# Performance work log

Hardware: AMD Instinct MI355X
Metric: run time of the kernel (lower is better)

Reference implementation:

```python
import jax, jax.numpy as jnp
import numpy as np

NUM_GROUPS = 5
EPS = 1e-5
QB = 128.0  # 2**(8-1) for b=8 activation quantization


def _binarize_weights_groupwise(W):
    """Sign-binarize W group-wise along out-feature dim, STE on backward.
    Faithful to torch: rows beyond num_groups*group_size remain zero."""
    n_out = W.shape[0]
    gs = n_out // NUM_GROUPS
    Wb = jnp.zeros_like(W)
    for g in range(NUM_GROUPS):  # small fixed loop (5 groups)
        wg = W[g * gs:(g + 1) * gs]
        z = wg - wg.mean()
        # STE: forward = sign(z), backward = identity w.r.t. z
        ste = z + jax.lax.stop_gradient(jnp.sign(z) - z)
        Wb = Wb.at[g * gs:(g + 1) * gs].set(ste)
    return Wb


def _quantize_activations_groupwise(x):
    """8-bit absmax quantization group-wise along dim 0 (batch), per torch code."""
    n = x.shape[0]
    gs = n // NUM_GROUPS
    xq = jnp.zeros_like(x)
    for g in range(NUM_GROUPS):
        ag = x[g * gs:(g + 1) * gs]
        gamma = jnp.max(jnp.abs(ag))
        xq = xq.at[g * gs:(g + 1) * gs].set(
            jnp.clip(ag * QB / (gamma + EPS), -QB + EPS, QB - EPS))
    return xq


def _bitlinear(x, W, b):
    Wb = _binarize_weights_groupwise(W)
    y = jnp.einsum('btc,oc->bto', x, Wb) + b
    return _quantize_activations_groupwise(y)


def setup_inputs() -> dict:
    key = jax.random.key(0)
    k1, k2, k3, k4, k5 = jax.random.split(key, 5)
    B, T, C = 10, 2048, 384
    H = 4 * C
    lim1 = 1.0 / np.sqrt(C)
    lim2 = 1.0 / np.sqrt(H)
    x = jax.random.normal(k1, (B, T, C), dtype=jnp.float32)
    W1 = jax.random.uniform(k2, (H, C), minval=-lim1, maxval=lim1, dtype=jnp.float32)
    b1 = jax.random.uniform(k3, (H,), minval=-lim1, maxval=lim1, dtype=jnp.float32)
    W2 = jax.random.uniform(k4, (C, H), minval=-lim2, maxval=lim2, dtype=jnp.float32)
    b2 = jax.random.uniform(k5, (C,), minval=-lim2, maxval=lim2, dtype=jnp.float32)
    return {"x": x, "W1": W1, "b1": b1, "W2": W2, "b2": b2}


def reference(x, W1, b1, W2, b2):
    h = _bitlinear(x, W1, b1)           # [B,T,4C], quantized to [-128,128]
    h = jax.nn.gelu(h, approximate=False)  # torch nn.GELU default is exact
    out = _bitlinear(h, W2, b2)         # [B,T,C]
    return out  # nn.Dropout is identity in eval/reference mode
```

## Files before the change

kernel.cpp:

```cpp
#include <hip/hip_runtime.h>
#include <cstdint>
#include <cstddef>

#define THREADS 256
#define NB 8

typedef float f32x4 __attribute__((ext_vector_type(4)));
typedef __bf16 bf16x8 __attribute__((ext_vector_type(8)));
typedef __bf16 bf16x4 __attribute__((ext_vector_type(4)));

__device__ __forceinline__ void gload_lds16(const void* g, void* l) {
    auto gp = (const __attribute__((address_space(1))) unsigned int*)(unsigned long long)(uintptr_t)g;
    auto lp = (__attribute__((address_space(3))) unsigned int*)(unsigned int)(uintptr_t)l;
    __builtin_amdgcn_global_load_lds(gp, lp, 16, 0, 0);
}

__device__ __forceinline__ float gelu_fast(float f) {
    const float z = f * 0.70710678118654752f;
    const float az = fabsf(z);
    const float t = __builtin_amdgcn_rcpf(fmaf(0.3275911f, az, 1.0f));
    float poly = fmaf(1.061405429f, t, -1.453152027f);
    poly = fmaf(poly, t, 1.421413741f);
    poly = fmaf(poly, t, -0.284496736f);
    poly = fmaf(poly, t, 0.254829592f);
    poly *= t;
    const float e = __builtin_amdgcn_exp2f(-az * az * 1.44269504088896f);
    float erfv = fmaf(-poly, e, 1.0f);
    erfv = copysignf(erfv, z);
    return 0.5f * f * (1.0f + erfv);
}

__global__ void prep_a(const float* __restrict__ x, __bf16* __restrict__ xb,
                       const float* __restrict__ W1, const float* __restrict__ W2,
                       float* __restrict__ partials, int epg1, int epg2,
                       unsigned int* __restrict__ gzero) {
    const int blk = blockIdx.x, tid = threadIdx.x;
    if (blk < 80) {
        const int y = blk >> 3, b = blk & 7;
        if (blk == 0 && tid < 16) gzero[tid] = 0u;
        const int epg = (y < 5) ? epg1 : epg2;
        const float* Wg = (y < 5) ? (W1 + (size_t)y * epg1)
                                  : (W2 + (size_t)(y - 5) * epg2);
        const int chunk4 = epg / (4 * NB);
        const float* base = Wg + (size_t)b * chunk4 * 4;
        float s = 0.f;
        for (int i = tid; i < chunk4; i += THREADS) {
            f32x4 v = *reinterpret_cast<const f32x4*>(base + 4 * (size_t)i);
            s += (v[0] + v[1]) + (v[2] + v[3]);
        }
        __shared__ float red[THREADS];
        red[tid] = s;
        __syncthreads();
        for (int off = THREADS / 2; off > 0; off >>= 1) {
            if (tid < off) red[tid] += red[tid + off];
            __syncthreads();
        }
        if (tid == 0) partials[y * NB + b] = red[0];
        return;
    }
    const int i = (blk - 80) * THREADS + tid;
    f32x4 v = *reinterpret_cast<const f32x4*>(x + 4 * (size_t)i);
    bf16x4 o;
    o[0] = (__bf16)v[0]; o[1] = (__bf16)v[1];
    o[2] = (__bf16)v[2]; o[3] = (__bf16)v[3];
    *reinterpret_cast<bf16x4*>(xb + 4 * (size_t)i) = o;
}

__global__ void prep_b(const float* __restrict__ W1, __bf16* __restrict__ W1b,
                       const float* __restrict__ W2, __bf16* __restrict__ W2b,
                       const float* __restrict__ psums,
                       int epg1, int tail1, int epg2, int tail2) {
    int r = blockIdx.x;
    const int tid = threadIdx.x;
    const float* W; __bf16* Wb; const float* ps; int epg, tail;
    if (r <= 40) { W = W1; Wb = W1b; ps = psums;      epg = epg1; tail = tail1; }
    else { r -= 41; W = W2; Wb = W2b; ps = psums + 40; epg = epg2; tail = tail2; }
    if (r == 40) {
        __bf16* og = Wb + (size_t)5 * epg;
        for (int i = tid; i < tail; i += THREADS) og[i] = (__bf16)0.f;
        return;
    }
    const int g = r >> 3, b = r & 7;
    float total = 0.f;
#pragma unroll
    for (int j = 0; j < NB; ++j) total += ps[g * NB + j];
    const float mean = total / (float)epg;
    const int chunk4 = epg / (4 * NB);
    const size_t off0 = (size_t)g * epg + (size_t)b * chunk4 * 4;
    const float* base = W + off0;
    __bf16* ob = Wb + off0;
    for (int i = tid; i < chunk4; i += THREADS) {
        f32x4 v = *reinterpret_cast<const f32x4*>(base + 4 * (size_t)i);
        bf16x4 o;
#pragma unroll
        for (int j = 0; j < 4; ++j) {
            const float z = v[j] - mean;
            o[j] = (__bf16)((z > 0.f) ? 1.f : ((z < 0.f) ? -1.f : 0.f));
        }
        *reinterpret_cast<bf16x4*>(ob + 4 * (size_t)i) = o;
    }
}

__global__ __launch_bounds__(512, 2)
void gemm1_bt(const __bf16* __restrict__ A, const __bf16* __restrict__ Bw,
              const float* __restrict__ bias, __bf16* __restrict__ outp,
              unsigned int* __restrict__ gmax, int M, int N, int K,
              int GN, int nwg) {
    constexpr int BM = 256, BN_ = 256, BK = 64, NF = 4;
    constexpr int ABYTES = BM * BK * 2;
    constexpr int BBYTES = BN_ * BK * 2;
    __shared__ __attribute__((aligned(16))) char lds[2 * (ABYTES + BBYTES)];

    const int tid = threadIdx.x;
    const int wave = tid >> 6, lane = tid & 63;
    const int l15 = lane & 15, l4 = lane >> 4;
    const int wr = wave >> 2, wc = wave & 3;

    const int cpx = nwg >> 3;
    const int orig = (blockIdx.x & 7) * cpx + (blockIdx.x >> 3);
    const int bm = orig / GN, bn = orig % GN;

    const __bf16* Ab = A + (size_t)bm * BM * K;
    const __bf16* Bb = Bw + (size_t)bn * BN_ * K;
    const int NT = K / BK;

    f32x4 acc[8][NF];
#pragma unroll
    for (int m = 0; m < 8; ++m)
#pragma unroll
        for (int n = 0; n < NF; ++n)
            acc[m][n] = f32x4{0.f, 0.f, 0.f, 0.f};

    auto STAGE = [&](int t) {
        const int k0 = t * BK;
        char* ab = lds + (t & 1) * (ABYTES + BBYTES);
        char* bb = ab + ABYTES;
#pragma unroll
        for (int j = 0; j < 4; ++j) {
            const int q = j * 8192 + tid * 16;
            const int lr = q >> 7;
            const int s = ((q >> 4) & 7) ^ (lr & 7);
            gload_lds16(Ab + (size_t)lr * K + k0 + s * 8, ab + q);
        }
#pragma unroll
        for (int j = 0; j < 4; ++j) {
            const int q = j * 8192 + tid * 16;
            const int lr = q >> 7;
            const int s = ((q >> 4) & 7) ^ (lr & 7);
            gload_lds16(Bb + (size_t)lr * K + k0 + s * 8, bb + q);
        }
    };

    STAGE(0);
    asm volatile("s_waitcnt vmcnt(0)" ::: "memory");
    __syncthreads();

    for (int t = 0; t < NT; ++t) {
        if (t + 1 < NT) STAGE(t + 1);
        const char* ab = lds + (t & 1) * (ABYTES + BBYTES);
        const char* bb = ab + ABYTES;
#pragma unroll
        for (int kk = 0; kk < 2; ++kk) {
            bf16x8 af[8], bfv[NF];
#pragma unroll
            for (int m = 0; m < 8; ++m) {
                const int r = wr * 128 + m * 16 + l15;
                const int sp = (kk * 4 + l4) ^ (r & 7);
                af[m] = *reinterpret_cast<const bf16x8*>(ab + r * 128 + sp * 16);
            }
#pragma unroll
            for (int n = 0; n < NF; ++n) {
                const int r = wc * 64 + n * 16 + l15;
                const int sp = (kk * 4 + l4) ^ (r & 7);
                bfv[n] = *reinterpret_cast<const bf16x8*>(bb + r * 128 + sp * 16);
            }
#pragma unroll
            for (int m = 0; m < 8; ++m)
#pragma unroll
                for (int n = 0; n < NF; ++n)
                    acc[m][n] = __builtin_amdgcn_mfma_f32_16x16x32_bf16(
                        bfv[n], af[m], acc[m][n], 0, 0, 0);
        }
        asm volatile("s_waitcnt vmcnt(0)" ::: "memory");
        __syncthreads();
    }

    const int rowb = bm * BM + wr * 128;
    const int colb = bn * BN_ + wc * 64;
    float lmax = 0.f;
#pragma unroll
    for (int n = 0; n < NF; ++n) {
        const f32x4 bv = *reinterpret_cast<const f32x4*>(bias + colb + n * 16 + l4 * 4);
#pragma unroll
        for (int m = 0; m < 8; ++m) {
            const int row = rowb + m * 16 + l15;
            bf16x4 o;
#pragma unroll
            for (int r = 0; r < 4; ++r) {
                const float v = acc[m][n][r] + bv[r];
                lmax = fmaxf(lmax, fabsf(v));
                o[r] = (__bf16)v;
            }
            *reinterpret_cast<bf16x4*>(
                &outp[(size_t)row * N + colb + n * 16 + l4 * 4]) = o;
        }
    }
#pragma unroll
    for (int off = 32; off > 0; off >>= 1)
        lmax = fmaxf(lmax, __shfl_down(lmax, off, 64));
    float* wredmax = (float*)lds;
    if (lane == 0) wredmax[wave] = lmax;
    __syncthreads();
    if (tid == 0) {
        float bmax = wredmax[0];
#pragma unroll
        for (int w = 1; w < 8; ++w) bmax = fmaxf(bmax, wredmax[w]);
        atomicMax(gmax + (bm * BM) / 4096, __float_as_uint(bmax));
    }
}

__global__ __launch_bounds__(512, 2)
void gemm2_bt(const __bf16* __restrict__ A, const __bf16* __restrict__ Bw,
              const float* __restrict__ bias, float* __restrict__ outp,
              unsigned int* __restrict__ gmax, int M, int N, int K,
              int GN, int nwg) {
    constexpr int BM = 256, BN_ = 128, BK = 64, NF = 2;
    constexpr int ABYTES = BM * BK * 2;
    constexpr int BBYTES = BN_ * BK * 2;
    __shared__ __attribute__((aligned(16))) char lds[2 * (ABYTES + BBYTES)];

    const int tid = threadIdx.x;
    const int wave = tid >> 6, lane = tid & 63;
    const int l15 = lane & 15, l4 = lane >> 4;
    const int wr = wave >> 2, wc = wave & 3;

    const int cpx = nwg >> 3;
    const int orig = (blockIdx.x & 7) * cpx + (blockIdx.x >> 3);
    const int bm = orig / GN, bn = orig % GN;

    const __bf16* Ab = A + (size_t)bm * BM * K;
    const __bf16* Bb = Bw + (size_t)bn * BN_ * K;
    const int NT = K / BK;

    f32x4 acc[8][NF];
#pragma unroll
    for (int m = 0; m < 8; ++m)
#pragma unroll
        for (int n = 0; n < NF; ++n)
            acc[m][n] = f32x4{0.f, 0.f, 0.f, 0.f};

    auto STAGE = [&](int t) {
        const int k0 = t * BK;
        char* ab = lds + (t & 1) * (ABYTES + BBYTES);
        char* bb = ab + ABYTES;
#pragma unroll
        for (int j = 0; j < 4; ++j) {
            const int q = j * 8192 + tid * 16;
            const int lr = q >> 7;
            const int s = ((q >> 4) & 7) ^ (lr & 7);
            gload_lds16(Ab + (size_t)lr * K + k0 + s * 8, ab + q);
        }
#pragma unroll
        for (int j = 0; j < 2; ++j) {
            const int q = j * 8192 + tid * 16;
            const int lr = q >> 7;
            const int s = ((q >> 4) & 7) ^ (lr & 7);
            gload_lds16(Bb + (size_t)lr * K + k0 + s * 8, bb + q);
        }
    };

    STAGE(0);
    asm volatile("s_waitcnt vmcnt(0)" ::: "memory");
    __syncthreads();

    for (int t = 0; t < NT; ++t) {
        if (t + 1 < NT) STAGE(t + 1);
        const char* ab = lds + (t & 1) * (ABYTES + BBYTES);
        const char* bb = ab + ABYTES;
#pragma unroll
        for (int kk = 0; kk < 2; ++kk) {
            bf16x8 af[8], bfv[NF];
#pragma unroll
            for (int m = 0; m < 8; ++m) {
                const int r = wr * 128 + m * 16 + l15;
                const int sp = (kk * 4 + l4) ^ (r & 7);
                af[m] = *reinterpret_cast<const bf16x8*>(ab + r * 128 + sp * 16);
            }
#pragma unroll
            for (int n = 0; n < NF; ++n) {
                const int r = wc * 32 + n * 16 + l15;
                const int sp = (kk * 4 + l4) ^ (r & 7);
                bfv[n] = *reinterpret_cast<const bf16x8*>(bb + r * 128 + sp * 16);
            }
#pragma unroll
            for (int m = 0; m < 8; ++m)
#pragma unroll
                for (int n = 0; n < NF; ++n)
                    acc[m][n] = __builtin_amdgcn_mfma_f32_16x16x32_bf16(
                        bfv[n], af[m], acc[m][n], 0, 0, 0);
        }
        asm volatile("s_waitcnt vmcnt(0)" ::: "memory");
        __syncthreads();
    }

    const int rowb = bm * BM + wr * 128;
    const int colb = bn * BN_ + wc * 32;
    float lmax = 0.f;
#pragma unroll
    for (int n = 0; n < NF; ++n) {
        const f32x4 bv = *reinterpret_cast<const f32x4*>(bias + colb + n * 16 + l4 * 4);
#pragma unroll
        for (int m = 0; m < 8; ++m) {
            const int row = rowb + m * 16 + l15;
            f32x4 o;
#pragma unroll
            for (int r = 0; r < 4; ++r) {
                o[r] = acc[m][n][r] + bv[r];
                lmax = fmaxf(lmax, fabsf(o[r]));
            }
            *reinterpret_cast<f32x4*>(
                &outp[(size_t)row * N + colb + n * 16 + l4 * 4]) = o;
        }
    }
#pragma unroll
    for (int off = 32; off > 0; off >>= 1)
        lmax = fmaxf(lmax, __shfl_down(lmax, off, 64));
    float* wredmax = (float*)lds;
    if (lane == 0) wredmax[wave] = lmax;
    __syncthreads();
    if (tid == 0) {
        float bmax = wredmax[0];
#pragma unroll
        for (int w = 1; w < 8; ++w) bmax = fmaxf(bmax, wredmax[w]);
        atomicMax(gmax + (bm * BM) / 4096, __float_as_uint(bmax));
    }
}

__global__ void quant_gelu(__bf16* __restrict__ y, const unsigned int* __restrict__ gbits,
                           int perg8, int n8) {
    const int stride = gridDim.x * blockDim.x;
    for (int i = blockIdx.x * blockDim.x + threadIdx.x; i < n8; i += stride) {
        const int g = i / perg8;
        const float gamma = __uint_as_float(gbits[g]);
        const float s = 128.0f / (gamma + 1e-5f);
        bf16x8 v = *reinterpret_cast<const bf16x8*>(y + 8 * (size_t)i);
        bf16x8 o;
#pragma unroll
        for (int j = 0; j < 8; ++j) {
            float f = (float)v[j] * s;
            f = fminf(fmaxf(f, -128.0f + 1e-5f), 128.0f - 1e-5f);
            o[j] = (__bf16)gelu_fast(f);
        }
        *reinterpret_cast<bf16x8*>(y + 8 * (size_t)i) = o;
    }
}

__global__ void final_scale(float* __restrict__ y, const unsigned int* __restrict__ gbits,
                            int perg4, int n4) {
    int i = blockIdx.x * blockDim.x + threadIdx.x;
    if (i >= n4) return;
    const int g = i / perg4;
    const float gamma = __uint_as_float(gbits[g]);
    const float s = 128.0f / (gamma + 1e-5f);
    f32x4 v = *reinterpret_cast<const f32x4*>(y + 4 * (size_t)i);
    f32x4 o;
#pragma unroll
    for (int j = 0; j < 4; ++j)
        o[j] = fminf(fmaxf(v[j] * s, -128.0f + 1e-5f), 128.0f - 1e-5f);
    *reinterpret_cast<f32x4*>(y + 4 * (size_t)i) = o;
}

extern "C" void kernel_launch(void* const* d_in, const int* in_sizes, int n_in,
                              void* d_out, int out_size, void* d_ws, size_t ws_size,
                              hipStream_t stream) {
    const float* x  = (const float*)d_in[0];
    const float* W1 = (const float*)d_in[1];
    const float* b1 = (const float*)d_in[2];
    const float* W2 = (const float*)d_in[3];
    const float* b2 = (const float*)d_in[4];
    float* out = (float*)d_out;

    const int BB = 10, TT = 2048, C = 384, H = 1536;
    const int M = BB * TT;

    const int gs1 = H / 5;
    const int gs2 = C / 5;
    const int epg1 = gs1 * C;
    const int epg2 = gs2 * H;
    const int tail1 = (H - 5 * gs1) * C;
    const int tail2 = (C - 5 * gs2) * H;

    const size_t szW1b = (size_t)H * C * 2;
    const size_t szW2b = (size_t)C * H * 2;
    const size_t szXb  = (size_t)M * C * 2;
    const size_t szY1  = (size_t)M * H * 2;

    char* p = (char*)d_ws;
    __bf16* W1b = (__bf16*)p; p += szW1b;
    __bf16* W2b = (__bf16*)p; p += szW2b;
    __bf16* xb  = (__bf16*)p; p += szXb;
    __bf16* y1  = (__bf16*)p; p += szY1;
    unsigned int* gamma = (unsigned int*)p; p += 64;
    float* psums = (float*)p; p += 2 * 5 * NB * 4;
    if ((size_t)(p - (char*)d_ws) > ws_size) return;

    prep_a<<<7760, THREADS, 0, stream>>>(x, xb, W1, W2, psums, epg1, epg2, gamma);

    prep_b<<<82, THREADS, 0, stream>>>(W1, W1b, W2, W2b, psums,
                                       epg1, tail1, epg2, tail2);

    gemm1_bt<<<480, 512, 0, stream>>>(
        xb, W1b, b1, y1, gamma, M, H, C, H / 256, 480);

    quant_gelu<<<2048, THREADS, 0, stream>>>(
        y1, gamma, (M / 5) * H / 8, M * H / 8);

    gemm2_bt<<<240, 512, 0, stream>>>(
        y1, W2b, b2, out, gamma + 5, M, C, H, C / 128, 240);

    final_scale<<<(M * C / 4 + THREADS - 1) / THREADS, THREADS, 0, stream>>>(
        out, gamma + 5, (M / 5) * C / 4, M * C / 4);
}
```

Measured before the change: 131.3 us.

## Merge GEMM kernels into templated triple-buffered pipeline with smaller N tile

Replaces the two separate GEMM kernels with one templated kernel that triple-buffers LDS and prefetches two K-tiles ahead, using partial vmcnt waits so global loads overlap more compute. GEMM1 now uses a 256x128 tile (960 workgroups instead of 480) instead of 256x256. Launch bounds drop to one block per CU because of the larger LDS footprint. The aim is to hide memory latency and balance load, at the cost of lower occupancy and more A-tile reloads for GEMM1.

```diff
diff --git a/kernel.cpp b/kernel.cpp
--- a/kernel.cpp
+++ b/kernel.cpp
@@ -101,15 +101,17 @@
     }
 }
 
-__global__ __launch_bounds__(512, 2)
-void gemm1_bt(const __bf16* __restrict__ A, const __bf16* __restrict__ Bw,
-              const float* __restrict__ bias, __bf16* __restrict__ outp,
-              unsigned int* __restrict__ gmax, int M, int N, int K,
-              int GN, int nwg) {
-    constexpr int BM = 256, BN_ = 256, BK = 64, NF = 4;
+template<int OUT_BF16>
+__global__ __launch_bounds__(512, 1)
+void gemm_p3(const __bf16* __restrict__ A, const __bf16* __restrict__ Bw,
+             const float* __restrict__ bias, void* __restrict__ outp,
+             unsigned int* __restrict__ gmax, int M, int N, int K,
+             int GN, int nwg) {
+    constexpr int BM = 256, BN_ = 128, BK = 64, NF = 2;
     constexpr int ABYTES = BM * BK * 2;
     constexpr int BBYTES = BN_ * BK * 2;
-    __shared__ __attribute__((aligned(16))) char lds[2 * (ABYTES + BBYTES)];
+    constexpr int BUF = ABYTES + BBYTES;
+    __shared__ __attribute__((aligned(16))) char lds[3 * BUF];
 
     const int tid = threadIdx.x;
     const int wave = tid >> 6, lane = tid & 63;
@@ -131,9 +133,9 @@
         for (int n = 0; n < NF; ++n)
             acc[m][n] = f32x4{0.f, 0.f, 0.f, 0.f};
 
-    auto STAGE = [&](int t) {
+    auto STAGE = [&](int t, int buf) {
         const int k0 = t * BK;
-        char* ab = lds + (t & 1) * (ABYTES + BBYTES);
+        char* ab = lds + buf * BUF;
         char* bb = ab + ABYTES;
 #pragma unroll
         for (int j = 0; j < 4; ++j) {
@@ -143,7 +145,7 @@
             gload_lds16(Ab + (size_t)lr * K + k0 + s * 8, ab + q);
         }
 #pragma unroll
-        for (int j = 0; j < 4; ++j) {
+        for (int j = 0; j < 2; ++j) {
             const int q = j * 8192 + tid * 16;
             const int lr = q >> 7;
             const int s = ((q >> 4) & 7) ^ (lr & 7);
@@ -151,13 +153,16 @@
         }
     };
 
-    STAGE(0);
-    asm volatile("s_waitcnt vmcnt(0)" ::: "memory");
+    STAGE(0, 0);
+    STAGE(1, 1);
+    asm volatile("s_waitcnt vmcnt(6)" ::: "memory");
     __syncthreads();
 
+    int cur = 0;
     for (int t = 0; t < NT; ++t) {
-        if (t + 1 < NT) STAGE(t + 1);
-        const char* ab = lds + (t & 1) * (ABYTES + BBYTES);
+        const int nxt2 = (cur >= 1) ? cur - 1 : cur + 2;
+        if (t + 2 < NT) STAGE(t + 2, nxt2);
+        const char* ab = lds + cur * BUF;
         const char* bb = ab + ABYTES;
 #pragma unroll
         for (int kk = 0; kk < 2; ++kk) {
@@ -170,124 +175,6 @@
             }
 #pragma unroll
             for (int n = 0; n < NF; ++n) {
-                const int r = wc * 64 + n * 16 + l15;
-                const int sp = (kk * 4 + l4) ^ (r & 7);
-                bfv[n] = *reinterpret_cast<const bf16x8*>(bb + r * 128 + sp * 16);
-            }
-#pragma unroll
-            for (int m = 0; m < 8; ++m)
-#pragma unroll
-                for (int n = 0; n < NF; ++n)
-                    acc[m][n] = __builtin_amdgcn_mfma_f32_16x16x32_bf16(
-                        bfv[n], af[m], acc[m][n], 0, 0, 0);
-        }
-        asm volatile("s_waitcnt vmcnt(0)" ::: "memory");
-        __syncthreads();
-    }
-
-    const int rowb = bm * BM + wr * 128;
-    const int colb = bn * BN_ + wc * 64;
-    float lmax = 0.f;
-#pragma unroll
-    for (int n = 0; n < NF; ++n) {
-        const f32x4 bv = *reinterpret_cast<const f32x4*>(bias + colb + n * 16 + l4 * 4);
-#pragma unroll
-        for (int m = 0; m < 8; ++m) {
-            const int row = rowb + m * 16 + l15;
-            bf16x4 o;
-#pragma unroll
-            for (int r = 0; r < 4; ++r) {
-                const float v = acc[m][n][r] + bv[r];
-                lmax = fmaxf(lmax, fabsf(v));
-                o[r] = (__bf16)v;
-            }
-            *reinterpret_cast<bf16x4*>(
-                &outp[(size_t)row * N + colb + n * 16 + l4 * 4]) = o;
-        }
-    }
-#pragma unroll
-    for (int off = 32; off > 0; off >>= 1)
-        lmax = fmaxf(lmax, __shfl_down(lmax, off, 64));
-    float* wredmax = (float*)lds;
-    if (lane == 0) wredmax[wave] = lmax;
-    __syncthreads();
-    if (tid == 0) {
-        float bmax = wredmax[0];
-#pragma unroll
-        for (int w = 1; w < 8; ++w) bmax = fmaxf(bmax, wredmax[w]);
-        atomicMax(gmax + (bm * BM) / 4096, __float_as_uint(bmax));
-    }
-}
-
-__global__ __launch_bounds__(512, 2)
-void gemm2_bt(const __bf16* __restrict__ A, const __bf16* __restrict__ Bw,
-              const float* __restrict__ bias, float* __restrict__ outp,
-              unsigned int* __restrict__ gmax, int M, int N, int K,
-              int GN, int nwg) {
-    constexpr int BM = 256, BN_ = 128, BK = 64, NF = 2;
-    constexpr int ABYTES = BM * BK * 2;
-    constexpr int BBYTES = BN_ * BK * 2;
-    __shared__ __attribute__((aligned(16))) char lds[2 * (ABYTES + BBYTES)];
-
-    const int tid = threadIdx.x;
-    const int wave = tid >> 6, lane = tid & 63;
-    const int l15 = lane & 15, l4 = lane >> 4;
-    const int wr = wave >> 2, wc = wave & 3;
-
-    const int cpx = nwg >> 3;
-    const int orig = (blockIdx.x & 7) * cpx + (blockIdx.x >> 3);
-    const int bm = orig / GN, bn = orig % GN;
-
-    const __bf16* Ab = A + (size_t)bm * BM * K;
-    const __bf16* Bb = Bw + (size_t)bn * BN_ * K;
-    const int NT = K / BK;
-
-    f32x4 acc[8][NF];
-#pragma unroll
-    for (int m = 0; m < 8; ++m)
-#pragma unroll
-        for (int n = 0; n < NF; ++n)
-            acc[m][n] = f32x4{0.f, 0.f, 0.f, 0.f};
-
-    auto STAGE = [&](int t) {
-        const int k0 = t * BK;
-        char* ab = lds + (t & 1) * (ABYTES + BBYTES);
-        char* bb = ab + ABYTES;
-#pragma unroll
-        for (int j = 0; j < 4; ++j) {
-            const int q = j * 8192 + tid * 16;
-            const int lr = q >> 7;
-            const int s = ((q >> 4) & 7) ^ (lr & 7);
-            gload_lds16(Ab + (size_t)lr * K + k0 + s * 8, ab + q);
-        }
-#pragma unroll
-        for (int j = 0; j < 2; ++j) {
-            const int q = j * 8192 + tid * 16;
-            const int lr = q >> 7;
-            const int s = ((q >> 4) & 7) ^ (lr & 7);
-            gload_lds16(Bb + (size_t)lr * K + k0 + s * 8, bb + q);
-        }
-    };
-
-    STAGE(0);
-    asm volatile("s_waitcnt vmcnt(0)" ::: "memory");
-    __syncthreads();
-
-    for (int t = 0; t < NT; ++t) {
-        if (t + 1 < NT) STAGE(t + 1);
-        const char* ab = lds + (t & 1) * (ABYTES + BBYTES);
-        const char* bb = ab + ABYTES;
-#pragma unroll
-        for (int kk = 0; kk < 2; ++kk) {
-            bf16x8 af[8], bfv[NF];
-#pragma unroll
-            for (int m = 0; m < 8; ++m) {
-                const int r = wr * 128 + m * 16 + l15;
-                const int sp = (kk * 4 + l4) ^ (r & 7);
-                af[m] = *reinterpret_cast<const bf16x8*>(ab + r * 128 + sp * 16);
-            }
-#pragma unroll
-            for (int n = 0; n < NF; ++n) {
                 const int r = wc * 32 + n * 16 + l15;
                 const int sp = (kk * 4 + l4) ^ (r & 7);
                 bfv[n] = *reinterpret_cast<const bf16x8*>(bb + r * 128 + sp * 16);
@@ -299,8 +186,10 @@
                     acc[m][n] = __builtin_amdgcn_mfma_f32_16x16x32_bf16(
                         bfv[n], af[m], acc[m][n], 0, 0, 0);
         }
-        asm volatile("s_waitcnt vmcnt(0)" ::: "memory");
+        if (t + 2 < NT)      asm volatile("s_waitcnt vmcnt(6)" ::: "memory");
+        else if (t + 1 < NT) asm volatile("s_waitcnt vmcnt(0)" ::: "memory");
         __syncthreads();
+        cur = (cur == 2) ? 0 : cur + 1;
     }
 
     const int rowb = bm * BM + wr * 128;
@@ -312,14 +201,26 @@
 #pragma unroll
         for (int m = 0; m < 8; ++m) {
             const int row = rowb + m * 16 + l15;
-            f32x4 o;
-#pragma unroll
-            for (int r = 0; r < 4; ++r) {
-                o[r] = acc[m][n][r] + bv[r];
-                lmax = fmaxf(lmax, fabsf(o[r]));
+            if (OUT_BF16) {
+                bf16x4 o;
+#pragma unroll
+                for (int r = 0; r < 4; ++r) {
+                    const float v = acc[m][n][r] + bv[r];
+                    lmax = fmaxf(lmax, fabsf(v));
+                    o[r] = (__bf16)v;
+                }
+                *reinterpret_cast<bf16x4*>(
+                    &((__bf16*)outp)[(size_t)row * N + colb + n * 16 + l4 * 4]) = o;
+            } else {
+                f32x4 o;
+#pragma unroll
+                for (int r = 0; r < 4; ++r) {
+                    o[r] = acc[m][n][r] + bv[r];
+                    lmax = fmaxf(lmax, fabsf(o[r]));
+                }
+                *reinterpret_cast<f32x4*>(
+                    &((float*)outp)[(size_t)row * N + colb + n * 16 + l4 * 4]) = o;
             }
-            *reinterpret_cast<f32x4*>(
-                &outp[(size_t)row * N + colb + n * 16 + l4 * 4]) = o;
         }
     }
 #pragma unroll
@@ -409,14 +310,14 @@
     prep_b<<<82, THREADS, 0, stream>>>(W1, W1b, W2, W2b, psums,
                                        epg1, tail1, epg2, tail2);
 
-    gemm1_bt<<<480, 512, 0, stream>>>(
-        xb, W1b, b1, y1, gamma, M, H, C, H / 256, 480);
+    gemm_p3<1><<<960, 512, 0, stream>>>(
+        xb, W1b, b1, (void*)y1, gamma, M, H, C, H / 128, 960);
 
     quant_gelu<<<2048, THREADS, 0, stream>>>(
         y1, gamma, (M / 5) * H / 8, M * H / 8);
 
-    gemm2_bt<<<240, 512, 0, stream>>>(
-        y1, W2b, b2, out, gamma + 5, M, C, H, C / 128, 240);
+    gemm_p3<0><<<240, 512, 0, stream>>>(
+        y1, W2b, b2, (void*)out, gamma + 5, M, C, H, C / 128, 240);
 
     final_scale<<<(M * C / 4 + THREADS - 1) / THREADS, THREADS, 0, stream>>>(
         out, gamma + 5, (M / 5) * C / 4, M * C / 4);
```

After: 139.0 us. 1.06x slower.
